# Kernel tuning notes

Measured on AMD Instinct MI355X. Metric: run time of the kernel, lower is better.

Reference implementation:

```python
import jax, jax.numpy as jnp
import numpy as np

D_MODEL = 1024
NUM_HEADS = 16
D_K = D_MODEL // NUM_HEADS


def setup_inputs() -> dict:
    key = jax.random.key(0)
    ks = jax.random.split(key, 11)
    B, S = 2, 2048
    s = 1.0 / np.sqrt(D_MODEL)
    return {
        "q": jax.random.normal(ks[0], (B, S, D_MODEL), jnp.float32),
        "k": jax.random.normal(ks[1], (B, S, D_MODEL), jnp.float32),
        "v": jax.random.normal(ks[2], (B, S, D_MODEL), jnp.float32),
        "w_q": jax.random.normal(ks[3], (D_MODEL, D_MODEL), jnp.float32) * s,
        "b_q": jnp.zeros((D_MODEL,), jnp.float32),
        "w_k": jax.random.normal(ks[4], (D_MODEL, D_MODEL), jnp.float32) * s,
        "b_k": jnp.zeros((D_MODEL,), jnp.float32),
        "w_v": jax.random.normal(ks[5], (D_MODEL, D_MODEL), jnp.float32) * s,
        "b_v": jnp.zeros((D_MODEL,), jnp.float32),
        "w_o": jax.random.normal(ks[6], (D_MODEL, D_MODEL), jnp.float32) * s,
        "b_o": jnp.zeros((D_MODEL,), jnp.float32),
    }


def reference(q, k, v, w_q, b_q, w_k, b_k, w_v, b_v, w_o, b_o):
    B, S, _ = q.shape
    H, Dk = NUM_HEADS, D_K

    def split_heads(x):  # [B,S,D] -> [B,H,S,Dk]
        return x.reshape(B, S, H, Dk).transpose(0, 2, 1, 3)

    # torch nn.Linear: x @ W.T + b
    qh = split_heads(q @ w_q.T + b_q)
    kh = split_heads(k @ w_k.T + b_k)
    vh = split_heads(v @ w_v.T + b_v)

    scale = 1.0 / jnp.sqrt(jnp.asarray(Dk, qh.dtype))
    scores = jnp.einsum("bhsd,bhtd->bhst", qh, kh) * scale  # [B,H,S,S]
    attn = jax.nn.softmax(scores, axis=-1)
    # dropout is identity in eval/deterministic baseline
    out = jnp.einsum("bhst,bhtd->bhsd", attn, vh)  # [B,H,S,Dk]
    out = out.transpose(0, 2, 1, 3).reshape(B, S, H * Dk)
    return out @ w_o.T + b_o
```

## Files before the change

### kernel.cpp

```cpp
#include <hip/hip_runtime.h>
#include <hip/hip_bf16.h>
#include <stdint.h>

typedef unsigned short u16;
typedef __attribute__((ext_vector_type(8))) short short8;
typedef __attribute__((ext_vector_type(8))) __bf16 bf16x8;
typedef __attribute__((ext_vector_type(4))) float f32x4;
typedef __attribute__((ext_vector_type(4))) uint32_t u32x4;

#if defined(__has_builtin)
#if __has_builtin(__builtin_amdgcn_global_load_lds)
#define USE_GLLDS 1
#endif
#endif

#if defined(__has_builtin)
#if __has_builtin(__builtin_amdgcn_exp2f)
#define HAVE_EXP2_BUILTIN 1
#endif
#endif
__device__ __forceinline__ float fexp2(float x) {
#ifdef HAVE_EXP2_BUILTIN
  return __builtin_amdgcn_exp2f(x);
#else
  return exp2f(x);
#endif
}

__device__ __forceinline__ u16 f2bf(float f) {
  __hip_bfloat16 h = __float2bfloat16(f);
  return __builtin_bit_cast(u16, h);
}

__device__ __forceinline__ uint32_t cvt_pk_bf16(float lo, float hi) {
  uint32_t w;
  asm("v_cvt_pk_bf16_f32 %0, %1, %2" : "=v"(w) : "v"(lo), "v"(hi));
  return w;
}

__device__ __forceinline__ f32x4 mfma16(bf16x8 a, bf16x8 b, f32x4 c) {
  return __builtin_amdgcn_mfma_f32_16x16x32_bf16(a, b, c, 0, 0, 0);
}

#ifdef USE_GLLDS
__device__ __forceinline__ void async_cp16(const void* g, void* l) {
  __builtin_amdgcn_global_load_lds(
      (const __attribute__((address_space(1))) void*)g,
      (__attribute__((address_space(3))) void*)l, 16, 0, 0);
}
#endif

__global__ __launch_bounds__(256) void cvt_all(
    const float* __restrict__ q, const float* __restrict__ k,
    const float* __restrict__ v, const float* __restrict__ w0,
    const float* __restrict__ w1, const float* __restrict__ w2,
    const float* __restrict__ w3, u16* __restrict__ dst) {
  size_t i = ((size_t)blockIdx.x * 256 + threadIdx.x) * 8;
  const size_t M1 = 1u << 20;
  const float* s;
  size_t base;
  if (i < 4 * M1) { s = q; base = 0; }
  else if (i < 8 * M1) { s = k; base = 4 * M1; }
  else if (i < 12 * M1) { s = v; base = 8 * M1; }
  else if (i < 13 * M1) { s = w0; base = 12 * M1; }
  else if (i < 14 * M1) { s = w1; base = 13 * M1; }
  else if (i < 15 * M1) { s = w2; base = 14 * M1; }
  else { s = w3; base = 15 * M1; }
  const float4 a = *(const float4*)(s + (i - base));
  const float4 b = *(const float4*)(s + (i - base) + 4);
  short8 r;
  r[0] = (short)f2bf(a.x); r[1] = (short)f2bf(a.y);
  r[2] = (short)f2bf(a.z); r[3] = (short)f2bf(a.w);
  r[4] = (short)f2bf(b.x); r[5] = (short)f2bf(b.y);
  r[6] = (short)f2bf(b.z); r[7] = (short)f2bf(b.w);
  *(short8*)(dst + i) = r;
}

__device__ __forceinline__ void gemm_core8(const u16* __restrict__ X,
                                           const u16* __restrict__ W,
                                           const float* __restrict__ bias,
                                           void* __restrict__ outp, int mode,
                                           int m0, int n0) {
  __shared__ u16 Al[128 * 64];
  __shared__ u16 Bl[128 * 64];
  const int tid = threadIdx.x;
  const int wv = tid >> 6, l = tid & 63;
  const int wr = wv >> 2, wc = wv & 3;
  const int lrow = l & 15, lk = (l >> 4) * 8;

  f32x4 acc[4][2];
#pragma unroll
  for (int i = 0; i < 4; ++i)
#pragma unroll
    for (int j = 0; j < 2; ++j) acc[i][j] = (f32x4){0.f, 0.f, 0.f, 0.f};

  const int srow = l >> 3;
  const int scol = (l & 7) * 8;
  const u16* Asrc = X + (size_t)(m0 + wv * 8 + srow) * 1024 + scol;
  const u16* Bsrc = W + (size_t)(wv * 8 + srow) * 1024 + scol;

  for (int kt = 0; kt < 1024; kt += 64) {
#ifdef USE_GLLDS
    async_cp16(Asrc + kt, &Al[(wv * 8) * 64]);
    async_cp16(Asrc + (size_t)64 * 1024 + kt, &Al[(wv * 8 + 64) * 64]);
    async_cp16(Bsrc + kt, &Bl[(wv * 8) * 64]);
    async_cp16(Bsrc + (size_t)64 * 1024 + kt, &Bl[(wv * 8 + 64) * 64]);
#else
    short8 a0 = *(const short8*)(Asrc + kt);
    short8 a1 = *(const short8*)(Asrc + (size_t)64 * 1024 + kt);
    short8 b0 = *(const short8*)(Bsrc + kt);
    short8 b1 = *(const short8*)(Bsrc + (size_t)64 * 1024 + kt);
    *(short8*)&Al[(wv * 8 + srow) * 64 + scol] = a0;
    *(short8*)&Al[(wv * 8 + 64 + srow) * 64 + scol] = a1;
    *(short8*)&Bl[(wv * 8 + srow) * 64 + scol] = b0;
    *(short8*)&Bl[(wv * 8 + 64 + srow) * 64 + scol] = b1;
#endif
    __syncthreads();
#pragma unroll
    for (int ks = 0; ks < 2; ++ks) {
      bf16x8 af[4], bf[2];
#pragma unroll
      for (int mf = 0; mf < 4; ++mf)
        af[mf] = *(const bf16x8*)&Al[(wr * 64 + mf * 16 + lrow) * 64 +
                                     ks * 32 + lk];
#pragma unroll
      for (int nf = 0; nf < 2; ++nf)
        bf[nf] = *(const bf16x8*)&Bl[(wc * 32 + nf * 16 + lrow) * 64 +
                                     ks * 32 + lk];
#pragma unroll
      for (int mf = 0; mf < 4; ++mf)
#pragma unroll
        for (int nf = 0; nf < 2; ++nf)
          acc[mf][nf] = mfma16(af[mf], bf[nf], acc[mf][nf]);
    }
    __syncthreads();
  }

  const int rb = (l >> 4) * 4;
#pragma unroll
  for (int mf = 0; mf < 4; ++mf) {
#pragma unroll
    for (int nf = 0; nf < 2; ++nf) {
      const int gn = n0 + wc * 32 + nf * 16 + lrow;
      const float bi = bias[gn];
#pragma unroll
      for (int r = 0; r < 4; ++r) {
        const int gm = m0 + wr * 64 + mf * 16 + rb + r;
        float val = acc[mf][nf][r] + bi;
        const int b = gm >> 11, s = gm & 2047, h = gn >> 6, d = gn & 63;
        if (mode == 3) {
          ((float*)outp)[(size_t)gm * 1024 + gn] = val;
        } else if (mode == 2) {
          ((u16*)outp)[(((size_t)((b * 16 + h) * 64 + d)) << 11) + s] = f2bf(val);
        } else {
          if (mode == 0) val *= 0.18033688f;
          ((u16*)outp)[(((size_t)((b * 16 + h) * 2048 + s)) << 6) + d] = f2bf(val);
        }
      }
    }
  }
}

__global__ __launch_bounds__(512, 6) void gemm_proj(
    const u16* __restrict__ qb, const u16* __restrict__ wqb,
    const float* __restrict__ b_q, const float* __restrict__ b_k,
    const float* __restrict__ b_v, u16* __restrict__ Qh) {
  const int s = blockIdx.x;
  const int xcd = s & 7, c = s >> 3;
  const int nx = (xcd >> 2) * 12 + (c % 12);
  const int my = (xcd & 3) * 8 + (c / 12);
  const int z = nx >> 3, nxl = nx & 7;
  const float* bias = (z == 0) ? b_q : ((z == 1) ? b_k : b_v);
  gemm_core8(qb + ((size_t)z << 22), wqb + ((size_t)nx << 17), bias,
             Qh + ((size_t)z << 22), z, my * 128, nxl * 128);
}

__global__ __launch_bounds__(512, 6) void gemm_out(
    const u16* __restrict__ X, const u16* __restrict__ W,
    const float* __restrict__ bias, float* __restrict__ out) {
  const int s = blockIdx.x;
  const int xcd = s & 7, c = s >> 3;
  const int nx = (xcd >> 2) * 4 + (c & 3);
  const int my = (xcd & 3) * 8 + (c >> 2);
  gemm_core8(X, W + ((size_t)nx << 17), bias, out, 3, my * 128, nx * 128);
}

__global__ __launch_bounds__(512, 4) void flash_attn5(
    const u16* __restrict__ Qh, const u16* __restrict__ Kh,
    const u16* __restrict__ VT, u16* __restrict__ Op,
    float2* __restrict__ ml) {
  __shared__ __align__(16) u16 Kbuf[4096];
  __shared__ __align__(16) u16 Vbuf[4096];
  __shared__ __align__(16) uint32_t Pl[8 * 576];

  const int tid = threadIdx.x;
  const int wv = tid >> 6, l = tid & 63;
  const int q = l & 15, g = l >> 4;

  const int s_lin = blockIdx.x + (blockIdx.y << 4) + (blockIdx.z << 9);
  const int o = ((s_lin & 7) << 7) + (s_lin >> 3);
  const int qt = o & 15, bh = (o >> 4) & 31, z = o >> 9;

  const u16* Qp = Qh + ((size_t)bh * 2048 + qt * 128 + wv * 16) * 64;
  const u16* Kp = Kh + (size_t)bh * 2048 * 64;
  const u16* Vp = VT + (size_t)bh * 64 * 2048;

  bf16x8 qf[2];
  qf[0] = *(const bf16x8*)(Qp + q * 64 + g * 8);
  qf[1] = *(const bf16x8*)(Qp + q * 64 + 32 + g * 8);

  f32x4 o_acc[4];
#pragma unroll
  for (int df = 0; df < 4; ++df) o_acc[df] = (f32x4){0.f, 0.f, 0.f, 0.f};
  float m = -1e30f, ls = 0.f;

  const int srow = l >> 3;
  const int scolq = (l & 7) ^ srow;
  const int pbase = wv * 576 + q * 36;
  const char* kb = (const char*)&Kbuf[0];
  const char* vb = (const char*)&Vbuf[0];
  const int rsw = (q & 7) << 4;

  const u16* kg = Kp + (size_t)(z * 1024 + wv * 8 + srow) * 64 + scolq * 8;
  const u16* vg = Vp + (size_t)(wv * 8 + srow) * 2048 + z * 1024 + scolq * 8;

  {
    short8 k0 = *(const short8*)kg;
    short8 v0 = *(const short8*)vg;
    *(short8*)&Kbuf[wv * 512 + l * 8] = k0;
    *(short8*)&Vbuf[wv * 512 + l * 8] = v0;
  }
  kg += 64 * 64;
  vg += 64;
  __syncthreads();

  for (int tt = 0; tt < 16; ++tt) {
    short8 kr, vr;
    if (tt < 15) {
      kr = *(const short8*)kg;
      vr = *(const short8*)vg;
      kg += 64 * 64;
      vg += 64;
    }

    f32x4 s[4];
#pragma unroll
    for (int nj = 0; nj < 4; ++nj) s[nj] = (f32x4){0.f, 0.f, 0.f, 0.f};
#pragma unroll
    for (int ks = 0; ks < 2; ++ks) {
#pragma unroll
      for (int nj = 0; nj < 4; ++nj) {
        bf16x8 kf = *(const bf16x8*)(kb + (nj * 16 + q) * 128 +
                                     (((ks * 4 + g) << 4) ^ rsw));
        s[nj] = mfma16(kf, qf[ks], s[nj]);
      }
    }

    const float a0 = fmaxf(fmaxf(s[0][0], s[0][1]), fmaxf(s[0][2], s[0][3]));
    const float a1 = fmaxf(fmaxf(s[1][0], s[1][1]), fmaxf(s[1][2], s[1][3]));
    const float a2 = fmaxf(fmaxf(s[2][0], s[2][1]), fmaxf(s[2][2], s[2][3]));
    const float a3 = fmaxf(fmaxf(s[3][0], s[3][1]), fmaxf(s[3][2], s[3][3]));
    float mt = fmaxf(fmaxf(a0, a1), fmaxf(a2, a3));
    mt = fmaxf(mt, __shfl_xor(mt, 16));
    mt = fmaxf(mt, __shfl_xor(mt, 32));
    if (!__all(mt <= m + 8.f)) {
      const float nm = fmaxf(m, mt);
      const float rf = fexp2(m - nm);
      m = nm;
      ls *= rf;
#pragma unroll
      for (int df = 0; df < 4; ++df) o_acc[df] *= rf;
    }
    float ps = 0.f;
#pragma unroll
    for (int nj = 0; nj < 4; ++nj)
#pragma unroll
      for (int r = 0; r < 4; ++r) {
        s[nj][r] = fexp2(s[nj][r] - m);
        ps += s[nj][r];
      }
    ps += __shfl_xor(ps, 16);
    ps += __shfl_xor(ps, 32);
    ls += ps;

#pragma unroll
    for (int nj = 0; nj < 4; ++nj)
#pragma unroll
      for (int pp = 0; pp < 2; ++pp)
        Pl[pbase + nj * 8 + g * 2 + pp] =
            cvt_pk_bf16(s[nj][2 * pp], s[nj][2 * pp + 1]);

#pragma unroll
    for (int ks = 0; ks < 2; ++ks) {
      u32x4 pw = *(const u32x4*)&Pl[pbase + ks * 16 + 4 * g];
      bf16x8 pf = __builtin_bit_cast(bf16x8, pw);
#pragma unroll
      for (int df = 0; df < 4; ++df) {
        bf16x8 vf = *(const bf16x8*)(vb + (df * 16 + q) * 128 +
                                     (((ks * 4 + g) << 4) ^ rsw));
        o_acc[df] = mfma16(vf, pf, o_acc[df]);
      }
    }

    __syncthreads();
    if (tt < 15) {
      *(short8*)&Kbuf[wv * 512 + l * 8] = kr;
      *(short8*)&Vbuf[wv * 512 + l * 8] = vr;
    }
    __syncthreads();
  }

  const float inv = 1.f / ls;
  const int rowb = qt * 128 + wv * 16 + q;
  const size_t prow = (size_t)(z * 32 + bh) * 2048 + rowb;
  u16* Po = Op + (prow << 6);
#pragma unroll
  for (int df = 0; df < 4; ++df)
#pragma unroll
    for (int pp = 0; pp < 2; ++pp) {
      uint32_t w = cvt_pk_bf16(o_acc[df][2 * pp] * inv,
                               o_acc[df][2 * pp + 1] * inv);
      *(uint32_t*)(Po + df * 16 + 4 * g + 2 * pp) = w;
    }
  if (g == 0) ml[prow] = make_float2(m, ls);
}

__global__ __launch_bounds__(256) void combine(
    const uint32_t* __restrict__ Op32, const float2* __restrict__ ml,
    u16* __restrict__ AO) {
  const int j = blockIdx.x * 256 + threadIdx.x;
  const int rowid = j >> 5, w5 = j & 31;
  const float2 a = ml[rowid];
  const float2 c = ml[(1 << 16) + rowid];
  const float M = fmaxf(a.x, c.x);
  float w1 = a.y * fexp2(a.x - M);
  float w2 = c.y * fexp2(c.x - M);
  const float inv = 1.f / (w1 + w2);
  w1 *= inv;
  w2 *= inv;
  const uint32_t p1 = Op32[j];
  const uint32_t p2 = Op32[(1u << 21) + j];
  const float lo = w1 * __builtin_bit_cast(float, p1 << 16) +
                   w2 * __builtin_bit_cast(float, p2 << 16);
  const float hi = w1 * __builtin_bit_cast(float, p1 & 0xffff0000u) +
                   w2 * __builtin_bit_cast(float, p2 & 0xffff0000u);
  const uint32_t outw = cvt_pk_bf16(lo, hi);
  const int bh = rowid >> 11, s = rowid & 2047, b = bh >> 4, h = bh & 15;
  ((uint32_t*)AO)[((size_t)(b * 2048 + s) << 9) + h * 32 + w5] = outw;
}

extern "C" void kernel_launch(void* const* d_in, const int* in_sizes, int n_in,
                              void* d_out, int out_size, void* d_ws,
                              size_t ws_size, hipStream_t stream) {
  const float* q = (const float*)d_in[0];
  const float* k = (const float*)d_in[1];
  const float* v = (const float*)d_in[2];
  const float* w_q = (const float*)d_in[3];
  const float* b_q = (const float*)d_in[4];
  const float* w_k = (const float*)d_in[5];
  const float* b_k = (const float*)d_in[6];
  const float* w_v = (const float*)d_in[7];
  const float* b_v = (const float*)d_in[8];
  const float* w_o = (const float*)d_in[9];
  const float* b_o = (const float*)d_in[10];

  u16* ws = (u16*)d_ws;
  u16* qb = ws;
  u16* wqb = ws + (12u << 20);
  u16* wob = ws + (15u << 20);
  u16* Qh = ws + (16u << 20);
  u16* Kh = ws + (20u << 20);
  u16* VT = ws + (24u << 20);
  u16* AO = ws + (28u << 20);
  u16* Op = ws;
  float2* ml = (float2*)(ws + (8u << 20));

  cvt_all<<<dim3(8192), dim3(256), 0, stream>>>(q, k, v, w_q, w_k, w_v, w_o, ws);
  gemm_proj<<<dim3(768), dim3(512), 0, stream>>>(qb, wqb, b_q, b_k, b_v, Qh);
  flash_attn5<<<dim3(16, 32, 2), dim3(512), 0, stream>>>(Qh, Kh, VT, Op, ml);
  combine<<<dim3(8192), dim3(256), 0, stream>>>((const uint32_t*)Op, ml, AO);
  gemm_out<<<dim3(256), dim3(512), 0, stream>>>(AO, wob, b_o, (float*)d_out);
}
```

Before: 163.0 us.

## Process two 64-key tiles per flash-attention iteration to halve barriers

```diff
diff --git a/kernel.cpp b/kernel.cpp
--- a/kernel.cpp
+++ b/kernel.cpp
@@ -185,12 +185,12 @@
   gemm_core8(X, W + ((size_t)nx << 17), bias, out, 3, my * 128, nx * 128);
 }
 
-__global__ __launch_bounds__(512, 4) void flash_attn5(
+__global__ __launch_bounds__(512, 4) void flash_attn7(
     const u16* __restrict__ Qh, const u16* __restrict__ Kh,
     const u16* __restrict__ VT, u16* __restrict__ Op,
     float2* __restrict__ ml) {
-  __shared__ __align__(16) u16 Kbuf[4096];
-  __shared__ __align__(16) u16 Vbuf[4096];
+  __shared__ __align__(16) u16 Kbuf[2][4096];
+  __shared__ __align__(16) u16 Vbuf[2][4096];
   __shared__ __align__(16) uint32_t Pl[8 * 576];
 
   const int tid = threadIdx.x;
@@ -217,8 +217,10 @@
   const int srow = l >> 3;
   const int scolq = (l & 7) ^ srow;
   const int pbase = wv * 576 + q * 36;
-  const char* kb = (const char*)&Kbuf[0];
-  const char* vb = (const char*)&Vbuf[0];
+  const char* kb0 = (const char*)&Kbuf[0][0];
+  const char* kb1 = (const char*)&Kbuf[1][0];
+  const char* vb0 = (const char*)&Vbuf[0][0];
+  const char* vb1 = (const char*)&Vbuf[1][0];
   const int rsw = (q & 7) << 4;
 
   const u16* kg = Kp + (size_t)(z * 1024 + wv * 8 + srow) * 64 + scolq * 8;
@@ -226,41 +228,55 @@
 
   {
     short8 k0 = *(const short8*)kg;
+    short8 k1 = *(const short8*)(kg + 4096);
     short8 v0 = *(const short8*)vg;
-    *(short8*)&Kbuf[wv * 512 + l * 8] = k0;
-    *(short8*)&Vbuf[wv * 512 + l * 8] = v0;
+    short8 v1 = *(const short8*)(vg + 64);
+    *(short8*)&Kbuf[0][wv * 512 + l * 8] = k0;
+    *(short8*)&Kbuf[1][wv * 512 + l * 8] = k1;
+    *(short8*)&Vbuf[0][wv * 512 + l * 8] = v0;
+    *(short8*)&Vbuf[1][wv * 512 + l * 8] = v1;
   }
-  kg += 64 * 64;
-  vg += 64;
+  kg += 8192;
+  vg += 128;
   __syncthreads();
 
-  for (int tt = 0; tt < 16; ++tt) {
-    short8 kr, vr;
-    if (tt < 15) {
-      kr = *(const short8*)kg;
-      vr = *(const short8*)vg;
-      kg += 64 * 64;
-      vg += 64;
-    }
-
-    f32x4 s[4];
-#pragma unroll
-    for (int nj = 0; nj < 4; ++nj) s[nj] = (f32x4){0.f, 0.f, 0.f, 0.f};
+  for (int tt = 0; tt < 8; ++tt) {
+    short8 kr0, kr1, vr0, vr1;
+    if (tt < 7) {
+      kr0 = *(const short8*)kg;
+      kr1 = *(const short8*)(kg + 4096);
+      vr0 = *(const short8*)vg;
+      vr1 = *(const short8*)(vg + 64);
+      kg += 8192;
+      vg += 128;
+    }
+
+    f32x4 s0[4], s1[4];
+#pragma unroll
+    for (int nj = 0; nj < 4; ++nj) {
+      s0[nj] = (f32x4){0.f, 0.f, 0.f, 0.f};
+      s1[nj] = (f32x4){0.f, 0.f, 0.f, 0.f};
+    }
 #pragma unroll
     for (int ks = 0; ks < 2; ++ks) {
 #pragma unroll
       for (int nj = 0; nj < 4; ++nj) {
-        bf16x8 kf = *(const bf16x8*)(kb + (nj * 16 + q) * 128 +
-                                     (((ks * 4 + g) << 4) ^ rsw));
-        s[nj] = mfma16(kf, qf[ks], s[nj]);
-      }
-    }
-
-    const float a0 = fmaxf(fmaxf(s[0][0], s[0][1]), fmaxf(s[0][2], s[0][3]));
-    const float a1 = fmaxf(fmaxf(s[1][0], s[1][1]), fmaxf(s[1][2], s[1][3]));
-    const float a2 = fmaxf(fmaxf(s[2][0], s[2][1]), fmaxf(s[2][2], s[2][3]));
-    const float a3 = fmaxf(fmaxf(s[3][0], s[3][1]), fmaxf(s[3][2], s[3][3]));
-    float mt = fmaxf(fmaxf(a0, a1), fmaxf(a2, a3));
+        const int off = (nj * 16 + q) * 128 + (((ks * 4 + g) << 4) ^ rsw);
+        bf16x8 kf0 = *(const bf16x8*)(kb0 + off);
+        bf16x8 kf1 = *(const bf16x8*)(kb1 + off);
+        s0[nj] = mfma16(kf0, qf[ks], s0[nj]);
+        s1[nj] = mfma16(kf1, qf[ks], s1[nj]);
+      }
+    }
+
+    float mt = s0[0][0];
+#pragma unroll
+    for (int nj = 0; nj < 4; ++nj)
+#pragma unroll
+      for (int r = 0; r < 4; ++r) {
+        mt = fmaxf(mt, s0[nj][r]);
+        mt = fmaxf(mt, s1[nj][r]);
+      }
     mt = fmaxf(mt, __shfl_xor(mt, 16));
     mt = fmaxf(mt, __shfl_xor(mt, 32));
     if (!__all(mt <= m + 8.f)) {
@@ -276,8 +292,9 @@
     for (int nj = 0; nj < 4; ++nj)
 #pragma unroll
       for (int r = 0; r < 4; ++r) {
-        s[nj][r] = fexp2(s[nj][r] - m);
-        ps += s[nj][r];
+        s0[nj][r] = fexp2(s0[nj][r] - m);
+        s1[nj][r] = fexp2(s1[nj][r] - m);
+        ps += s0[nj][r] + s1[nj][r];
       }
     ps += __shfl_xor(ps, 16);
     ps += __shfl_xor(ps, 32);
@@ -288,24 +305,43 @@
 #pragma unroll
       for (int pp = 0; pp < 2; ++pp)
         Pl[pbase + nj * 8 + g * 2 + pp] =
-            cvt_pk_bf16(s[nj][2 * pp], s[nj][2 * pp + 1]);
-
+            cvt_pk_bf16(s0[nj][2 * pp], s0[nj][2 * pp + 1]);
 #pragma unroll
     for (int ks = 0; ks < 2; ++ks) {
       u32x4 pw = *(const u32x4*)&Pl[pbase + ks * 16 + 4 * g];
       bf16x8 pf = __builtin_bit_cast(bf16x8, pw);
 #pragma unroll
       for (int df = 0; df < 4; ++df) {
-        bf16x8 vf = *(const bf16x8*)(vb + (df * 16 + q) * 128 +
+        bf16x8 vf = *(const bf16x8*)(vb0 + (df * 16 + q) * 128 +
                                      (((ks * 4 + g) << 4) ^ rsw));
         o_acc[df] = mfma16(vf, pf, o_acc[df]);
       }
     }
 
+#pragma unroll
+    for (int nj = 0; nj < 4; ++nj)
+#pragma unroll
+      for (int pp = 0; pp < 2; ++pp)
+        Pl[pbase + nj * 8 + g * 2 + pp] =
+            cvt_pk_bf16(s1[nj][2 * pp], s1[nj][2 * pp + 1]);
+#pragma unroll
+    for (int ks = 0; ks < 2; ++ks) {
+      u32x4 pw = *(const u32x4*)&Pl[pbase + ks * 16 + 4 * g];
+      bf16x8 pf = __builtin_bit_cast(bf16x8, pw);
+#pragma unroll
+      for (int df = 0; df < 4; ++df) {
+        bf16x8 vf = *(const bf16x8*)(vb1 + (df * 16 + q) * 128 +
+                                     (((ks * 4 + g) << 4) ^ rsw));
+        o_acc[df] = mfma16(vf, pf, o_acc[df]);
+      }
+    }
+
     __syncthreads();
-    if (tt < 15) {
-      *(short8*)&Kbuf[wv * 512 + l * 8] = kr;
-      *(short8*)&Vbuf[wv * 512 + l * 8] = vr;
+    if (tt < 7) {
+      *(short8*)&Kbuf[0][wv * 512 + l * 8] = kr0;
+      *(short8*)&Kbuf[1][wv * 512 + l * 8] = kr1;
+      *(short8*)&Vbuf[0][wv * 512 + l * 8] = vr0;
+      *(short8*)&Vbuf[1][wv * 512 + l * 8] = vr1;
     }
     __syncthreads();
   }
@@ -377,7 +413,7 @@
 
   cvt_all<<<dim3(8192), dim3(256), 0, stream>>>(q, k, v, w_q, w_k, w_v, w_o, ws);
   gemm_proj<<<dim3(768), dim3(512), 0, stream>>>(qb, wqb, b_q, b_k, b_v, Qh);
-  flash_attn5<<<dim3(16, 32, 2), dim3(512), 0, stream>>>(Qh, Kh, VT, Op, ml);
+  flash_attn7<<<dim3(16, 32, 2), dim3(512), 0, stream>>>(Qh, Kh, VT, Op, ml);
   combine<<<dim3(8192), dim3(256), 0, stream>>>((const uint32_t*)Op, ml, AO);
   gemm_out<<<dim3(256), dim3(512), 0, stream>>>(AO, wob, b_o, (float*)d_out);
 }
```

Result: faster. 156.2 us (-4.2%).
